# Optimization experiments

Measured on AMD Instinct MI355X. Metric: run time of the kernel, lower is better.

## Reference

```python
import jax, jax.numpy as jnp
import numpy as np

# LDPC code / sim constants
N = 4096          # codeword length (pcm.shape[1])
M = 2048          # number of check nodes (pcm.shape[0])
DV = 3            # variable-node degree (regular code)
DC = 6            # check-node degree
E = N * DV        # number of Tanner-graph edges (== M * DC)
B = 2048          # batch_size arg of WeightedBP.call
NUM_ITER = 5      # self._num_iter (decoder run with num_iter=1, stateful, NUM_ITER times)
EBNO_DB = 4.0
CODERATE = 1.0 - M / N
EPS = 1e-12
ATANH_CLIP = 1.0 - 1e-7


def setup_inputs() -> dict:
    key = jax.random.key(0)
    k1, k2 = jax.random.split(key)
    rng = np.random.RandomState(0)
    # regular (3,6) Tanner graph: edge e connects vn_idx[e] <-> cn_idx[e]
    vn_idx = np.repeat(np.arange(N, dtype=np.int32), DV)                    # [E]
    cn_idx = rng.permutation(np.repeat(np.arange(M, dtype=np.int32), DC))   # [E]
    return {
        "noise_r": jax.random.normal(k1, (B, N), dtype=jnp.float32),
        "noise_i": jax.random.normal(k2, (B, N), dtype=jnp.float32),
        "edge_weights": jnp.ones((E,), dtype=jnp.float32),  # trainable per-edge BP weights, init 1
        "vn_idx": jnp.asarray(vn_idx),
        "cn_idx": jnp.asarray(cn_idx),
    }


def reference(noise_r, noise_i, edge_weights, vn_idx, cn_idx):
    # --- channel simulation (fading=False): c = 0, x = 1+0j, h = 1 ---
    no = 1.0 / (CODERATE * 2.0 * (10.0 ** (EBNO_DB / 10.0)))  # ebnodb2no, 2 bits/symbol
    n_std = jnp.sqrt(jnp.float32(no / 2.0))
    y_real = 1.0 + n_std * noise_r                 # Re(h*x + w); noise_i drops out of Re()
    del noise_i
    llr = 4.0 * y_real / jnp.float32(no)           # [B, N] channel LLRs (llr<0 -> bit 1)

    # --- stateful weighted BP, boxplus CN update, NUM_ITER unrolled iterations ---
    msg_vn = llr[:, vn_idx]                        # [B, E] initial VN->CN messages
    llr_total = llr
    for _ in range(NUM_ITER):
        mw = msg_vn * edge_weights[None, :]        # trainable weights on VN->CN messages
        t = jnp.tanh(mw * 0.5)                     # [B, E]
        logt = jnp.log(jnp.abs(t) + EPS)
        sgn = (t < 0.0).astype(jnp.float32)
        # per-check exclusive product in log/sign domain (scatter-add then subtract self)
        sum_log = jnp.zeros((B, M), jnp.float32).at[:, cn_idx].add(logt)
        sum_sgn = jnp.zeros((B, M), jnp.float32).at[:, cn_idx].add(sgn)
        excl_log = sum_log[:, cn_idx] - logt       # [B, E]
        excl_sgn = 1.0 - 2.0 * jnp.mod(sum_sgn[:, cn_idx] - sgn, 2.0)
        mag = jnp.clip(jnp.exp(excl_log), 0.0, ATANH_CLIP)
        msg_cn = excl_sgn * 2.0 * jnp.arctanh(mag)  # CN->VN messages [B, E]
        # VN update: marginal minus self
        sum_cn = jnp.zeros((B, N), jnp.float32).at[:, vn_idx].add(msg_cn)
        llr_total = llr + sum_cn                   # decoder soft output c_hat (hard: llr<0 -> 1)
        msg_vn = llr_total[:, vn_idx] - msg_cn
    return llr_total
```

## Files before the change

kernel.cpp:

```cpp
#include <hip/hip_runtime.h>
#include <math.h>

#define NV 4096
#define MC 2048
#define DV 3
#define DC 6
#define NE (NV * DV)
#define NB 2048
#define NITER 5
#define TPB 1024

__global__ __launch_bounds__(256) void build_cn(const int* __restrict__ cn_idx,
                                                int* __restrict__ cn_edges,
                                                int* __restrict__ cn_cnt) {
    int e = blockIdx.x * 256 + threadIdx.x;
    if (e < NE) {
        int m = cn_idx[e];
        int slot = atomicAdd(&cn_cnt[m], 1);
        cn_edges[m * DC + slot] = e;
    }
}

__global__ __launch_bounds__(256) void sort_cn(int* __restrict__ cn_edges) {
    int m = blockIdx.x * 256 + threadIdx.x;
    if (m < MC) {
        int v[DC];
        for (int j = 0; j < DC; ++j) v[j] = cn_edges[m * DC + j];
        for (int i = 1; i < DC; ++i) {
            int key = v[i]; int j = i - 1;
            while (j >= 0 && v[j] > key) { v[j + 1] = v[j]; --j; }
            v[j + 1] = key;
        }
        for (int j = 0; j < DC; ++j) cn_edges[m * DC + j] = v[j];
    }
}

static __device__ __forceinline__ float exp2_negabs(float x) {
    float r;
    asm volatile("v_exp_f32 %0, -abs(%1)" : "=v"(r) : "v"(x));
    return r;
}
static __device__ __forceinline__ float log2_raw(float x) {
    float r;
    asm volatile("v_log_f32 %0, %1" : "=v"(r) : "v"(x));
    return r;
}

__global__ __launch_bounds__(TPB, 8) void bp_iter(const float* __restrict__ noise_r,
                                                  const float* __restrict__ ew,
                                                  const int* __restrict__ cn_edges,
                                                  float* __restrict__ out) {
    __shared__ float msg[NE];
    const int b = blockIdx.x;
    const int t = threadIdx.x;

    const float NO    = (float)0.3981071705534972;
    const float NSTD  = sqrtf((float)(0.3981071705534972 * 0.5));
    const float LOG2E = 1.4426950408889634f;
    const float LN2   = 0.6931471805599453f;

    int idx[MC / TPB][DC];
#pragma unroll
    for (int c = 0; c < MC / TPB; ++c)
#pragma unroll
        for (int j = 0; j < DC; ++j)
            idx[c][j] = cn_edges[(t + TPB * c) * DC + j];

    float llr2[NV / TPB];
    const float* nb = noise_r + (size_t)b * NV;
#pragma unroll
    for (int k = 0; k < NV / TPB; ++k) {
        int n = t + TPB * k;
        float y  = 1.0f + NSTD * nb[n];
        float l  = (4.0f * y) / NO;
        float l2 = l * LOG2E;
        llr2[k] = l2;
        msg[3 * n + 0] = l2 * ew[3 * n + 0];
        msg[3 * n + 1] = l2 * ew[3 * n + 1];
        msg[3 * n + 2] = l2 * ew[3 * n + 2];
    }
    __syncthreads();

    for (int it = 0; it < NITER; ++it) {
#pragma unroll
        for (int c = 0; c < MC / TPB; ++c) {
            float a[DC], bb[DC], s[DC];
            float sprod = 1.0f;
#pragma unroll
            for (int j = 0; j < DC; ++j) {
                float mw = msg[idx[c][j]];
                s[j] = copysignf(1.0f, mw);
                sprod *= s[j];
                float u = exp2_negabs(mw);
                a[j]  = 1.0f + u;
                bb[j] = fmaxf(1.0f - u, 1e-12f);
            }

            float P = 1.0f, M = 1.0f;
#pragma unroll
            for (int j = 0; j < DC; ++j) {
                P *= a[j];
                M *= bb[j];
            }

#pragma unroll
            for (int j = 0; j < DC; ++j) {
                float Pb  = P * bb[j];
                float Ma  = M * a[j];
                float num = Pb + Ma;
                float den = fmaxf(Pb - Ma, 0x1.0p-23f * Pb);
                float val = log2_raw(__fdividef(num, den));
                msg[idx[c][j]] = val * (sprod * s[j]);
            }
        }
        __syncthreads();

        if (it < NITER - 1) {
#pragma unroll
            for (int k = 0; k < NV / TPB; ++k) {
                int n = t + TPB * k;
                float c0 = msg[3 * n + 0];
                float c1 = msg[3 * n + 1];
                float c2 = msg[3 * n + 2];
                float tot = llr2[k] + (c0 + c1 + c2);
                msg[3 * n + 0] = (tot - c0) * ew[3 * n + 0];
                msg[3 * n + 1] = (tot - c1) * ew[3 * n + 1];
                msg[3 * n + 2] = (tot - c2) * ew[3 * n + 2];
            }
            __syncthreads();
        } else {
#pragma unroll
            for (int k = 0; k < NV / TPB; ++k) {
                int n = t + TPB * k;
                float c0 = msg[3 * n + 0];
                float c1 = msg[3 * n + 1];
                float c2 = msg[3 * n + 2];
                out[(size_t)b * NV + n] = (llr2[k] + (c0 + c1 + c2)) * LN2;
            }
        }
    }
}

extern "C" void kernel_launch(void* const* d_in, const int* in_sizes, int n_in,
                              void* d_out, int out_size, void* d_ws, size_t ws_size,
                              hipStream_t stream) {
    const float* noise_r = (const float*)d_in[0];
    const float* ew      = (const float*)d_in[2];
    const int*   cn_idx  = (const int*)d_in[4];
    float* out = (float*)d_out;

    int* cn_edges = (int*)d_ws;
    int* cn_cnt   = cn_edges + NE;

    hipMemsetAsync(cn_cnt, 0, MC * sizeof(int), stream);
    build_cn<<<(NE + 255) / 256, 256, 0, stream>>>(cn_idx, cn_edges, cn_cnt);
    sort_cn<<<(MC + 255) / 256, 256, 0, stream>>>(cn_edges);
    bp_iter<<<NB, TPB, 0, stream>>>(noise_r, ew, cn_edges, out);
}
```

Baseline: 122.1 us.

## Reorder check-node edge slots to balance LDS banks and pack sign bits

Adds a preprocessing kernel that, for each wavefront's 64 check nodes, permutes the order of each check's six edge indices. It greedily picks the edge whose LDS bank (index mod 32) has been used least so far at each slot position, so the gathered shared-memory reads and writes in the CN update hit fewer bank conflicts. It also replaces float sign multiplications with a packed sign bitmask, popcount parity and bitwise sign insertion. This adds a small serial kernel launch per call. The sign change assumes val is non-negative, which holds because log2 of num/den is at least zero.

```diff
diff --git a/kernel.cpp b/kernel.cpp
--- a/kernel.cpp
+++ b/kernel.cpp
@@ -32,6 +32,33 @@
             v[j + 1] = key;
         }
         for (int j = 0; j < DC; ++j) cn_edges[m * DC + j] = v[j];
+    }
+}
+
+__global__ void balance_cn(int* __restrict__ cn_edges) {
+    __shared__ int counts[16][DC][32];
+    const int w = threadIdx.x;
+    const int c = blockIdx.x;
+    for (int j = 0; j < DC; ++j)
+        for (int k = 0; k < 32; ++k) counts[w][j][k] = 0;
+    for (int l = 0; l < 64; ++l) {
+        int* row = cn_edges + (w * 64 + l + c * TPB) * DC;
+        int e[DC];
+        for (int j = 0; j < DC; ++j) e[j] = row[j];
+        unsigned used = 0;
+        for (int j = 0; j < DC; ++j) {
+            int best = 0, bestCnt = 1 << 30, bestE = 1 << 30;
+            for (int q = 0; q < DC; ++q) {
+                if (used & (1u << q)) continue;
+                int cnt = counts[w][j][e[q] & 31];
+                if (cnt < bestCnt || (cnt == bestCnt && e[q] < bestE)) {
+                    bestCnt = cnt; best = q; bestE = e[q];
+                }
+            }
+            used |= 1u << best;
+            row[j] = e[best];
+            counts[w][j][e[best] & 31]++;
+        }
     }
 }
 
@@ -72,8 +99,7 @@
     for (int k = 0; k < NV / TPB; ++k) {
         int n = t + TPB * k;
         float y  = 1.0f + NSTD * nb[n];
-        float l  = (4.0f * y) / NO;
-        float l2 = l * LOG2E;
+        float l2 = ((4.0f * y) / NO) * LOG2E;
         llr2[k] = l2;
         msg[3 * n + 0] = l2 * ew[3 * n + 0];
         msg[3 * n + 1] = l2 * ew[3 * n + 1];
@@ -84,17 +110,17 @@
     for (int it = 0; it < NITER; ++it) {
 #pragma unroll
         for (int c = 0; c < MC / TPB; ++c) {
-            float a[DC], bb[DC], s[DC];
-            float sprod = 1.0f;
+            float a[DC], bb[DC];
+            unsigned spack = 0u;
 #pragma unroll
             for (int j = 0; j < DC; ++j) {
                 float mw = msg[idx[c][j]];
-                s[j] = copysignf(1.0f, mw);
-                sprod *= s[j];
+                spack |= ((__float_as_uint(mw) >> 31) & 1u) << j;
                 float u = exp2_negabs(mw);
                 a[j]  = 1.0f + u;
                 bb[j] = fmaxf(1.0f - u, 1e-12f);
             }
+            const unsigned par = __popc(spack) & 1u;
 
             float P = 1.0f, M = 1.0f;
 #pragma unroll
@@ -110,7 +136,8 @@
                 float num = Pb + Ma;
                 float den = fmaxf(Pb - Ma, 0x1.0p-23f * Pb);
                 float val = log2_raw(__fdividef(num, den));
-                msg[idx[c][j]] = val * (sprod * s[j]);
+                msg[idx[c][j]] = __uint_as_float(__float_as_uint(val) |
+                                                 (((par ^ (spack >> j)) & 1u) << 31));
             }
         }
         __syncthreads();
@@ -155,5 +182,6 @@
     hipMemsetAsync(cn_cnt, 0, MC * sizeof(int), stream);
     build_cn<<<(NE + 255) / 256, 256, 0, stream>>>(cn_idx, cn_edges, cn_cnt);
     sort_cn<<<(MC + 255) / 256, 256, 0, stream>>>(cn_edges);
+    balance_cn<<<MC / TPB, TPB / 64, 0, stream>>>(cn_edges);
     bp_iter<<<NB, TPB, 0, stream>>>(noise_r, ew, cn_edges, out);
 }
```

Measured after the change: 338.4 us. 2.77x slower.
